# Kernel optimization log

Measured on AMD Instinct MI355X. Metric: run time of the kernel, lower is better.

## Reference

```python
import jax, jax.numpy as jnp
import numpy as np

D_MODEL = 1024
N_HEADS = 16  # long-term branch; short/medium use N_HEADS // 2


def _band_bias(seq_len, scale_factor):
    # Intended semantics of create_temporal_mask: position i may attend to
    # positions j >= i - scale_factor (recent past + all future); positions
    # further than scale_factor in the past are blocked.
    i = jnp.arange(seq_len)[:, None]
    j = jnp.arange(seq_len)[None, :]
    return jnp.where(j >= i - scale_factor, 0.0, -1e9).astype(jnp.float32)


def _mha(x, w_in, b_in, w_out, b_out, n_heads, bias):
    # Faithful nn.MultiheadAttention (batch_first, eval/no dropout).
    B, S, D = x.shape
    dk = D // n_heads
    qkv = x @ w_in.T + b_in                       # [B,S,3D]
    q, k, v = jnp.split(qkv, 3, axis=-1)
    def heads(t):
        return t.reshape(B, S, n_heads, dk).transpose(0, 2, 1, 3)  # [B,H,S,dk]
    q, k, v = heads(q), heads(k), heads(v)
    scores = jnp.einsum('bhid,bhjd->bhij', q, k) / np.sqrt(dk).astype(np.float32)
    if bias is not None:
        scores = scores + bias
    attn = jax.nn.softmax(scores, axis=-1)        # [B,H,S,S]
    out = jnp.einsum('bhij,bhjd->bhid', attn, v)  # [B,H,S,dk]
    out = out.transpose(0, 2, 1, 3).reshape(B, S, D)
    return out @ w_out.T + b_out, attn


def _layernorm(x, gamma, beta, eps=1e-5):
    mu = jnp.mean(x, axis=-1, keepdims=True)
    var = jnp.var(x, axis=-1, keepdims=True)
    return (x - mu) * jax.lax.rsqrt(var + eps) * gamma + beta


def setup_inputs() -> dict:
    key = jax.random.key(0)
    ks = jax.random.split(key, 12)
    D = D_MODEL
    s = 0.02
    inp = {
        'x': jax.random.normal(ks[0], (2, 2048, D), dtype=jnp.float32),
        'w_in_s': jax.random.normal(ks[1], (3 * D, D), dtype=jnp.float32) * s,
        'b_in_s': jnp.zeros((3 * D,), dtype=jnp.float32),
        'wo_s': jax.random.normal(ks[2], (D, D), dtype=jnp.float32) * s,
        'bo_s': jnp.zeros((D,), dtype=jnp.float32),
        'w_in_m': jax.random.normal(ks[3], (3 * D, D), dtype=jnp.float32) * s,
        'b_in_m': jnp.zeros((3 * D,), dtype=jnp.float32),
        'wo_m': jax.random.normal(ks[4], (D, D), dtype=jnp.float32) * s,
        'bo_m': jnp.zeros((D,), dtype=jnp.float32),
        'w_in_l': jax.random.normal(ks[5], (3 * D, D), dtype=jnp.float32) * s,
        'b_in_l': jnp.zeros((3 * D,), dtype=jnp.float32),
        'wo_l': jax.random.normal(ks[6], (D, D), dtype=jnp.float32) * s,
        'bo_l': jnp.zeros((D,), dtype=jnp.float32),
        'w_comb': jax.random.normal(ks[7], (D, 3 * D), dtype=jnp.float32) * s,
        'b_comb': jnp.zeros((D,), dtype=jnp.float32),
        'gamma': jnp.ones((D,), dtype=jnp.float32),
        'beta': jnp.zeros((D,), dtype=jnp.float32),
    }
    return inp


def reference(x, w_in_s, b_in_s, wo_s, bo_s,
              w_in_m, b_in_m, wo_m, bo_m,
              w_in_l, b_in_l, wo_l, bo_l,
              w_comb, b_comb, gamma, beta):
    B, S, D = x.shape
    short_bias = _band_bias(S, 10)
    medium_bias = _band_bias(S, 30)
    short_out, _ = _mha(x, w_in_s, b_in_s, wo_s, bo_s, N_HEADS // 2, short_bias)
    medium_out, _ = _mha(x, w_in_m, b_in_m, wo_m, bo_m, N_HEADS // 2, medium_bias)
    long_out, attn = _mha(x, w_in_l, b_in_l, wo_l, bo_l, N_HEADS, None)
    attn_weights = jnp.mean(attn, axis=1)  # torch default average_attn_weights=True -> [B,S,S]
    combined = jnp.concatenate([short_out, medium_out, long_out], axis=-1)
    output = combined @ w_comb.T + b_comb
    return _layernorm(output + x, gamma, beta), attn_weights
```

## Files before the change

kernel.cpp:

```cpp
#include <hip/hip_runtime.h>
#include <hip/hip_bf16.h>
#include <math.h>

#define B_ 2
#define S_ 2048
#define D_ 1024
#define M_ (B_*S_)
#define CTXLD 3072

typedef _Float16 half8_t __attribute__((ext_vector_type(8)));
typedef _Float16 half4_t __attribute__((ext_vector_type(4)));
typedef float    f32x4  __attribute__((ext_vector_type(4)));

#define GL2LDS(g, l) __builtin_amdgcn_global_load_lds( \
    (const __attribute__((address_space(1))) void*)(uintptr_t)(g), \
    (__attribute__((address_space(3))) void*)(l), 16, 0, 0)

#define QSC_L  0.18033688011112043f
#define QSC_SM 0.12751744653921766f

struct GemmBatch {
    const _Float16* A;
    const _Float16* W;
    const float*    bias;
    void*           C;
    void*           C2;
};

template<int MODE, int NB>
__global__ __launch_bounds__(256) void gemm_f16(
    GemmBatch b0, GemmBatch b1, GemmBatch b2, int lda, int ldw, int ldc, int K)
{
    constexpr int NT = NB / 32;
    __shared__ __align__(16) _Float16 As[2*128*32];
    __shared__ __align__(16) _Float16 Bs[2*NB*32];

    const GemmBatch G = (blockIdx.z == 0) ? b0 : ((blockIdx.z == 1) ? b1 : b2);

    const int t = threadIdx.x, lane = t & 63, w = t >> 6;
    const int bm = blockIdx.x * 128, bn = blockIdx.y * NB;
    const int wm = (w >> 1) * 64, wn = (w & 1) * (NB/2);
    const int fr = lane & 15, q8 = (lane >> 4) * 8;
    const int srow = lane >> 2, scol = (lane & 3) * 8;

    f32x4 acc[4][NT] = {};

    const _Float16* Ab = G.A + (size_t)(bm + w*32 + srow) * lda + scol;
    const _Float16* Wb = G.W + (size_t)(bn + w*(NB/4) + srow) * ldw + scol;

    for (int k0 = 0; k0 < K; k0 += 64) {
        __syncthreads();
        #pragma unroll
        for (int kc = 0; kc < 2; kc++) {
            #pragma unroll
            for (int ii = 0; ii < 2; ii++)
                GL2LDS(Ab + (size_t)(ii*16)*lda + k0 + kc*32,
                       As + kc*4096 + w*1024 + ii*512);
            #pragma unroll
            for (int ii = 0; ii < NB/64; ii++)
                GL2LDS(Wb + (size_t)(ii*16)*ldw + k0 + kc*32,
                       Bs + kc*NB*32 + w*(NB/4)*32 + ii*512);
        }
        __syncthreads();
        #pragma unroll
        for (int kc = 0; kc < 2; kc++) {
            half8_t af[4], bf[NT];
            #pragma unroll
            for (int mt = 0; mt < 4; mt++)
                af[mt] = *(const half8_t*)&As[kc*4096 + (wm + mt*16 + fr)*32 + q8];
            #pragma unroll
            for (int nt = 0; nt < NT; nt++)
                bf[nt] = *(const half8_t*)&Bs[kc*NB*32 + (wn + nt*16 + fr)*32 + q8];
            #pragma unroll
            for (int mt = 0; mt < 4; mt++)
                #pragma unroll
                for (int nt = 0; nt < NT; nt++)
                    acc[mt][nt] = __builtin_amdgcn_mfma_f32_16x16x32_f16(
                        af[mt], bf[nt], acc[mt][nt], 0, 0, 0);
        }
    }

    const int cl = lane & 15;
    const int rq = (lane >> 4) * 4;

    if (MODE == 2 && bn >= 2048) {
        #pragma unroll
        for (int mt = 0; mt < 4; mt++) {
            int row0 = bm + wm + mt*16 + rq;
            #pragma unroll
            for (int nt = 0; nt < NT; nt++) {
                int gcol = bn + wn + nt*16 + cl;
                float bv = G.bias[gcol];
                half4_t hv = {(_Float16)(acc[mt][nt][0] + bv),
                              (_Float16)(acc[mt][nt][1] + bv),
                              (_Float16)(acc[mt][nt][2] + bv),
                              (_Float16)(acc[mt][nt][3] + bv)};
                *(half4_t*)((_Float16*)G.C2 + (size_t)(gcol - 2048) * M_ + row0) = hv;
            }
        }
        return;
    }

    const float qsc = (MODE == 2 && bn < 1024)
                      ? ((blockIdx.z == 2) ? QSC_L : QSC_SM) : 1.0f;

    #pragma unroll
    for (int mt = 0; mt < 4; mt++) {
        #pragma unroll
        for (int r = 0; r < 4; r++) {
            size_t grow = (size_t)(bm + wm + mt*16 + rq + r);
            #pragma unroll
            for (int nt = 0; nt < NT; nt++) {
                int gcol = bn + wn + nt*16 + cl;
                float v = acc[mt][nt][r] + ((MODE == 3) ? 0.f : G.bias[gcol]);
                if (MODE == 2) v *= qsc;
                if (MODE == 0)
                    ((float*)G.C)[grow * ldc + gcol] = v;
                else
                    ((_Float16*)G.C)[grow * ldc + gcol] = (_Float16)v;
            }
        }
    }
}

struct CastArgs {
    const float* s[5];
    _Float16*    d[5];
    int          nb[5];
};

__global__ __launch_bounds__(256) void cast_all(CastArgs a)
{
    int off = blockIdx.x;
    int seg = 0;
    while (seg < 4 && off >= a.nb[seg]) { off -= a.nb[seg]; seg++; }
    int i = off * 256 + threadIdx.x;
    float4 v = ((const float4*)a.s[seg])[i];
    half4_t h = {(_Float16)v.x, (_Float16)v.y, (_Float16)v.z, (_Float16)v.w};
    ((half4_t*)a.d[seg])[i] = h;
}

__global__ __launch_bounds__(256) void transpose_cast_wo(
    const float* s0, const float* s1, const float* s2,
    _Float16* d0, _Float16* d1, _Float16* d2)
{
    __shared__ float T[64][68];
    const float* src = blockIdx.z == 0 ? s0 : (blockIdx.z == 1 ? s1 : s2);
    _Float16*    dst = blockIdx.z == 0 ? d0 : (blockIdx.z == 1 ? d1 : d2);
    const int db = blockIdx.x * 64;
    const int eb = blockIdx.y * 64;
    const int r = threadIdx.x >> 4;
    const int c = (threadIdx.x & 15) * 4;

    #pragma unroll
    for (int rr = 0; rr < 4; rr++) {
        float4 v = *(const float4*)&src[(size_t)(db + rr*16 + r)*1024 + eb + c];
        T[rr*16 + r][c+0] = v.x; T[rr*16 + r][c+1] = v.y;
        T[rr*16 + r][c+2] = v.z; T[rr*16 + r][c+3] = v.w;
    }
    __syncthreads();
    #pragma unroll
    for (int rr = 0; rr < 4; rr++) {
        int e = rr*16 + r;
        half4_t hv = {(_Float16)T[c+0][e], (_Float16)T[c+1][e],
                      (_Float16)T[c+2][e], (_Float16)T[c+3][e]};
        *(half4_t*)&dst[(size_t)(eb + e)*1024 + db + c] = hv;
    }
}

__global__ __launch_bounds__(256) void beff_kernel(
    const float* __restrict__ w_comb, const float* __restrict__ b_comb,
    const float* __restrict__ bo_s, const float* __restrict__ bo_m,
    const float* __restrict__ bo_l, float* __restrict__ beff)
{
    __shared__ float red[4];
    const int n = blockIdx.x, t = threadIdx.x;
    float s = 0.f;
    for (int d = t; d < 1024; d += 256)
        s += w_comb[(size_t)n*3072 + d]        * bo_s[d]
           + w_comb[(size_t)n*3072 + 1024 + d] * bo_m[d]
           + w_comb[(size_t)n*3072 + 2048 + d] * bo_l[d];
    #pragma unroll
    for (int m = 32; m >= 1; m >>= 1) s += __shfl_xor(s, m);
    if ((t & 63) == 0) red[t >> 6] = s;
    __syncthreads();
    if (t == 0) beff[n] = b_comb[n] + red[0] + red[1] + red[2] + red[3];
}

template<int DK, int BJ, bool LOUT>
__device__ __forceinline__ void flash_body(
    _Float16* lds, float* Lw,
    const _Float16* __restrict__ qk, const _Float16* __restrict__ vT,
    _Float16* __restrict__ ctx, float* __restrict__ lout,
    int window, int b, int h, int qblk, int H)
{
    constexpr int KS  = DK / 32;
    constexpr int DT  = DK / 16;
    constexpr int JT  = BJ / 16;
    constexpr int JC  = BJ / 32;
    constexpr int LDP = 40;

    _Float16* Ks = lds;
    _Float16* Vs = lds + DK*BJ;
    _Float16* Ps = lds + 2*DK*BJ;

    const int t = threadIdx.x, lane = t & 63, w = t >> 6;
    const int fr = lane & 15, g = lane >> 4, k8 = g * 8;
    const int k8s = (g ^ ((fr >> 1) & 3)) * 8;
    const int blkQ = qblk * 64;
    const int qlo  = blkQ + w * 16;

    _Float16* PsW = Ps + w * 16 * LDP;
    const int srow = lane >> 2;
    const int ssw  = ((lane & 3) ^ ((srow >> 1) & 3)) * 8;

    half8_t qf[KS];
    #pragma unroll
    for (int kk = 0; kk < KS; kk++)
        qf[kk] = *(const half8_t*)&qk[(size_t)(b*S_ + qlo + fr)*2048 + h*DK + kk*32 + k8];

    f32x4 O[DT] = {};
    float lsum = 0.f;

    for (int j0 = 0; j0 < S_; j0 += BJ) {
        if (window >= 0 && j0 + BJ - 1 < blkQ - window) continue;
        __syncthreads();

        #pragma unroll
        for (int kk = 0; kk < KS; kk++)
            #pragma unroll
            for (int ii = 0; ii < BJ/64; ii++)
                GL2LDS(&qk[(size_t)(b*S_ + j0 + w*(BJ/4) + ii*16 + srow)*2048
                           + 1024 + h*DK + kk*32 + ssw],
                       &Ks[kk*BJ*32 + w*(BJ/4)*32 + ii*512]);
        #pragma unroll
        for (int jc = 0; jc < JC; jc++)
            #pragma unroll
            for (int ii = 0; ii < DK/64; ii++)
                GL2LDS(&vT[(size_t)(h*DK + w*(DK/4) + ii*16 + srow)*M_
                           + b*S_ + j0 + jc*32 + ssw],
                       &Vs[jc*DK*32 + w*(DK/4)*32 + ii*512]);
        __syncthreads();

        f32x4 st[JT];
        #pragma unroll
        for (int jt = 0; jt < JT; jt++) {
            f32x4 s = {};
            #pragma unroll
            for (int kk = 0; kk < KS; kk++) {
                half8_t kf = *(const half8_t*)&Ks[kk*BJ*32 + (jt*16 + fr)*32 + k8s];
                s = __builtin_amdgcn_mfma_f32_16x16x32_f16(kf, qf[kk], s, 0, 0, 0);
            }
            st[jt] = s;
        }

        const bool full = (window < 0) || (j0 >= qlo + 15 - window);
        #pragma unroll
        for (int kc = 0; kc < JC; kc++) {
            #pragma unroll
            for (int jh = 0; jh < 2; jh++) {
                int jt = kc*2 + jh;
                float p[4];
                #pragma unroll
                for (int r = 0; r < 4; r++) {
                    float pv = exp2f(st[jt][r]);
                    if (!full) {
                        int jg = j0 + jt*16 + g*4 + r;
                        if (jg < (qlo + fr) - window) pv = 0.f;
                    }
                    p[r] = pv;
                    lsum += pv;
                }
                half4_t ph = {(_Float16)p[0], (_Float16)p[1],
                              (_Float16)p[2], (_Float16)p[3]};
                *(half4_t*)&PsW[fr*LDP + jh*16 + g*4] = ph;
            }
            half8_t pf = *(const half8_t*)&PsW[fr*LDP + k8];
            #pragma unroll
            for (int dt = 0; dt < DT; dt++) {
                half8_t vf = *(const half8_t*)&Vs[kc*DK*32 + (dt*16 + fr)*32 + k8s];
                O[dt] = __builtin_amdgcn_mfma_f32_16x16x32_f16(pf, vf, O[dt], 0, 0, 0);
            }
        }
    }

    lsum += __shfl_xor(lsum, 16);
    lsum += __shfl_xor(lsum, 32);
    if (g == 0) Lw[w*16 + fr] = lsum;
    float linv[4];
    #pragma unroll
    for (int r = 0; r < 4; r++)
        linv[r] = 1.f / Lw[w*16 + g*4 + r];

    if (LOUT && g == 0)
        lout[(size_t)(b*H + h)*S_ + qlo + fr] = lsum;

    #pragma unroll
    for (int r = 0; r < 4; r++) {
        _Float16* cp = ctx + (size_t)(b*S_ + qlo + g*4 + r)*CTXLD + h*DK;
        #pragma unroll
        for (int dt = 0; dt < DT; dt++)
            cp[dt*16 + fr] = (_Float16)(O[dt][r] * linv[r]);
    }
}

__global__ __launch_bounds__(256, 4) void flash_mega(
    const _Float16* __restrict__ qk_s, const _Float16* __restrict__ qk_m,
    const _Float16* __restrict__ qk_l,
    const _Float16* __restrict__ vT_s, const _Float16* __restrict__ vT_m,
    const _Float16* __restrict__ vT_l,
    _Float16* __restrict__ ctxall, float* __restrict__ lbuf)
{
    __shared__ __align__(16) _Float16 lds[18944];
    __shared__ float Lw[64];

    const int hwb = blockIdx.x;
    const int bid = (hwb & 7) * 256 + (hwb >> 3);
    if (bid < 1024) {
        int qblk = bid & 31, h = (bid >> 5) & 15, b = bid >> 9;
        flash_body<64, 128, true>(lds, Lw, qk_l, vT_l, ctxall + 2048, lbuf,
                                  -1, b, h, qblk, 16);
    } else {
        int r = bid - 1024;
        int qblk = r & 31;
        int h = (r >> 5) & 7;
        int z = r >> 8;
        int br = z >> 1, b = z & 1;
        flash_body<128, 64, false>(lds, Lw, br ? qk_m : qk_s, br ? vT_m : vT_s,
                                   ctxall + (br ? 1024 : 0), nullptr,
                                   br ? 30 : 10, b, h, qblk, 8);
    }
}

__global__ __launch_bounds__(256, 4) void attn_mean3(
    const _Float16* __restrict__ qk,
    const float* __restrict__ lbuf,
    float* __restrict__ attn)
{
    __shared__ __align__(16) _Float16 Ks[2 * 2 * 128 * 32];

    const int t = threadIdx.x, lane = t & 63, w = t >> 6;
    const int fr = lane & 15, g = lane >> 4, k8 = g * 8;
    const int k8s = (g ^ ((fr >> 1) & 3)) * 8;
    const int j0 = blockIdx.x * 128;
    const int irow = blockIdx.y * 64 + w * 16;
    const int b = blockIdx.z;
    const int srow = lane >> 2;
    const int ssw  = ((lane & 3) ^ ((srow >> 1) & 3)) * 8;

    f32x4 acc[8] = {};

    for (int hp = 0; hp < 16; hp += 2) {
        __syncthreads();
        #pragma unroll
        for (int hh = 0; hh < 2; hh++)
            #pragma unroll
            for (int kk = 0; kk < 2; kk++)
                #pragma unroll
                for (int ii = 0; ii < 2; ii++)
                    GL2LDS(&qk[(size_t)(b*S_ + j0 + w*32 + ii*16 + srow)*2048
                               + 1024 + (hp+hh)*64 + kk*32 + ssw],
                           &Ks[hh*8192 + kk*4096 + w*1024 + ii*512]);
        __syncthreads();

        #pragma unroll
        for (int hh = 0; hh < 2; hh++) {
            const int h = hp + hh;
            half8_t af[2];
            #pragma unroll
            for (int kk = 0; kk < 2; kk++)
                af[kk] = *(const half8_t*)
                    &qk[(size_t)(b*S_ + irow + fr)*2048 + h*64 + kk*32 + k8];

            float lg[4];
            #pragma unroll
            for (int r = 0; r < 4; r++)
                lg[r] = __log2f(lbuf[(size_t)(b*16 + h)*S_ + irow + g*4 + r]) + 4.0f;

            #pragma unroll
            for (int nt = 0; nt < 8; nt++) {
                f32x4 s = {};
                #pragma unroll
                for (int kk = 0; kk < 2; kk++) {
                    half8_t bf = *(const half8_t*)
                        &Ks[hh*8192 + kk*4096 + (nt*16 + fr)*32 + k8s];
                    s = __builtin_amdgcn_mfma_f32_16x16x32_f16(af[kk], bf, s, 0, 0, 0);
                }
                #pragma unroll
                for (int r = 0; r < 4; r++)
                    acc[nt][r] += exp2f(s[r] - lg[r]);
            }
        }
    }

    #pragma unroll
    for (int r = 0; r < 4; r++) {
        float* p = attn + (size_t)(b*S_ + irow + g*4 + r)*S_ + j0;
        #pragma unroll
        for (int nt = 0; nt < 8; nt++)
            p[nt*16 + fr] = acc[nt][r];
    }
}

__global__ __launch_bounds__(256) void ln_residual(
    const float* __restrict__ pre, const float* __restrict__ x,
    const float* __restrict__ gamma, const float* __restrict__ beta,
    float* __restrict__ out)
{
    __shared__ float redS[4], redQ[4];
    const int row = blockIdx.x;
    const int t = threadIdx.x;
    size_t base = (size_t)row * D_ + t * 4;

    float4 v  = *(const float4*)(pre + base);
    float4 xv = *(const float4*)(x + base);
    v.x += xv.x; v.y += xv.y; v.z += xv.z; v.w += xv.w;

    float s = v.x + v.y + v.z + v.w;
    float q = v.x*v.x + v.y*v.y + v.z*v.z + v.w*v.w;
    #pragma unroll
    for (int m = 32; m >= 1; m >>= 1) {
        s += __shfl_xor(s, m);
        q += __shfl_xor(q, m);
    }
    int wave = t >> 6;
    if ((t & 63) == 0) { redS[wave] = s; redQ[wave] = q; }
    __syncthreads();
    s = redS[0] + redS[1] + redS[2] + redS[3];
    q = redQ[0] + redQ[1] + redQ[2] + redQ[3];

    float mean = s * (1.f / D_);
    float var  = q * (1.f / D_) - mean * mean;
    float rstd = rsqrtf(var + 1e-5f);

    float4 g  = *(const float4*)(gamma + t * 4);
    float4 be = *(const float4*)(beta + t * 4);
    float4 o;
    o.x = (v.x - mean) * rstd * g.x + be.x;
    o.y = (v.y - mean) * rstd * g.y + be.y;
    o.z = (v.z - mean) * rstd * g.z + be.z;
    o.w = (v.w - mean) * rstd * g.w + be.w;
    *(float4*)(out + base) = o;
}

extern "C" void kernel_launch(void* const* d_in, const int* in_sizes, int n_in,
                              void* d_out, int out_size, void* d_ws, size_t ws_size,
                              hipStream_t stream)
{
    (void)in_sizes; (void)n_in; (void)out_size; (void)ws_size;
    const float* x      = (const float*)d_in[0];
    const float* w_in_s = (const float*)d_in[1];
    const float* b_in_s = (const float*)d_in[2];
    const float* wo_s   = (const float*)d_in[3];
    const float* bo_s   = (const float*)d_in[4];
    const float* w_in_m = (const float*)d_in[5];
    const float* b_in_m = (const float*)d_in[6];
    const float* wo_m   = (const float*)d_in[7];
    const float* bo_m   = (const float*)d_in[8];
    const float* w_in_l = (const float*)d_in[9];
    const float* b_in_l = (const float*)d_in[10];
    const float* wo_l   = (const float*)d_in[11];
    const float* bo_l   = (const float*)d_in[12];
    const float* w_comb = (const float*)d_in[13];
    const float* b_comb = (const float*)d_in[14];
    const float* gamma  = (const float*)d_in[15];
    const float* beta   = (const float*)d_in[16];

    float* out    = (float*)d_out;
    float* attn_o = out + (size_t)M_ * D_;

    char* W = (char*)d_ws;
    _Float16* w_in_s_h = (_Float16*)(W);
    _Float16* w_in_m_h = (_Float16*)(W + 6291456);
    _Float16* w_in_l_h = (_Float16*)(W + 12582912);
    _Float16* w_comb_h = (_Float16*)(W + 18874368);
    _Float16* woT_s    = (_Float16*)(W + 25165824);
    _Float16* woT_m    = (_Float16*)(W + 27262976);
    _Float16* woT_l    = (_Float16*)(W + 29360128);
    _Float16* weff     = (_Float16*)(W + 31457280);
    _Float16* qk_s     = (_Float16*)(W + 37748736);
    _Float16* qk_m     = (_Float16*)(W + 54525952);
    _Float16* qk_l     = (_Float16*)(W + 71303168);
    _Float16* vT_s     = (_Float16*)(W + 88080384);
    _Float16* vT_m     = (_Float16*)(W + 96468992);
    _Float16* ctxall   = (_Float16*)(W + 104857600);
    _Float16* x_h      = (_Float16*)(W + 130023424);
    float*    lbuf     = (float*)   (W + 138412032);
    float*    beff     = (float*)   (W + 138674432);
    _Float16* vT_l     = w_comb_h;
    float*    pre      = (float*)qk_m;

    dim3 blk(256);
    GemmBatch nil = { nullptr, nullptr, nullptr, nullptr, nullptr };

    CastArgs ca;
    ca.s[0]=x;      ca.d[0]=x_h;      ca.nb[0]=4096;
    ca.s[1]=w_in_s; ca.d[1]=w_in_s_h; ca.nb[1]=3072;
    ca.s[2]=w_in_m; ca.d[2]=w_in_m_h; ca.nb[2]=3072;
    ca.s[3]=w_in_l; ca.d[3]=w_in_l_h; ca.nb[3]=3072;
    ca.s[4]=w_comb; ca.d[4]=w_comb_h; ca.nb[4]=3072;
    cast_all<<<dim3(16384), blk, 0, stream>>>(ca);

    transpose_cast_wo<<<dim3(16, 16, 3), blk, 0, stream>>>(
        wo_s, wo_m, wo_l, woT_s, woT_m, woT_l);

    GemmBatch we0 = { w_comb_h + 0,    woT_s, nullptr, weff + 0,    nullptr };
    GemmBatch we1 = { w_comb_h + 1024, woT_m, nullptr, weff + 1024, nullptr };
    GemmBatch we2 = { w_comb_h + 2048, woT_l, nullptr, weff + 2048, nullptr };
    gemm_f16<3, 64><<<dim3(8, 16, 3), blk, 0, stream>>>(we0, we1, we2, 3072, 1024, 3072, 1024);

    beff_kernel<<<dim3(1024), blk, 0, stream>>>(w_comb, b_comb, bo_s, bo_m, bo_l, beff);

    GemmBatch qs = { x_h, w_in_s_h, b_in_s, qk_s, vT_s };
    GemmBatch qm = { x_h, w_in_m_h, b_in_m, qk_m, vT_m };
    GemmBatch ql = { x_h, w_in_l_h, b_in_l, qk_l, vT_l };
    gemm_f16<2, 128><<<dim3(M_/128, 3072/128, 3), blk, 0, stream>>>(qs, qm, ql, D_, D_, 2048, D_);

    flash_mega<<<dim3(2048), blk, 0, stream>>>(
        qk_s, qk_m, qk_l, vT_s, vT_m, vT_l, ctxall, lbuf);

    attn_mean3<<<dim3(S_/128, S_/64, B_), blk, 0, stream>>>(qk_l, lbuf, attn_o);

    GemmBatch fb = { ctxall, weff, beff, pre, nullptr };
    gemm_f16<0, 64><<<dim3(M_/128, 1024/64, 1), blk, 0, stream>>>(fb, nil, nil, 3072, 3072, D_, 3072);

    ln_residual<<<dim3(M_), blk, 0, stream>>>(pre, x, gamma, beta, out);
}
```

Before: 527.5 us.

## Merge prep kernels and co-schedule final GEMM with attention-mean kernel

Folds the cast, transpose-cast and effective-bias kernels into one prep launch dispatched by block index. It also runs the final combine GEMM and the attention-weight mean computation in a single tail launch that shares one LDS buffer. The aim is to cut launch overhead and let two independent workloads fill the GPU together instead of running back to back. The cost is that the tail kernel's LDS footprint and launch bounds now cover both bodies, which may change occupancy for the GEMM part.

```diff
diff --git a/kernel.cpp b/kernel.cpp
--- a/kernel.cpp
+++ b/kernel.cpp
@@ -28,17 +28,14 @@
 };
 
 template<int MODE, int NB>
-__global__ __launch_bounds__(256) void gemm_f16(
-    GemmBatch b0, GemmBatch b1, GemmBatch b2, int lda, int ldw, int ldc, int K)
+__device__ __forceinline__ void gemm_body(
+    _Float16* As, _Float16* Bs, const GemmBatch& G,
+    int lda, int ldw, int ldc, int K, int bx, int by, int bz)
 {
     constexpr int NT = NB / 32;
-    __shared__ __align__(16) _Float16 As[2*128*32];
-    __shared__ __align__(16) _Float16 Bs[2*NB*32];
-
-    const GemmBatch G = (blockIdx.z == 0) ? b0 : ((blockIdx.z == 1) ? b1 : b2);
 
     const int t = threadIdx.x, lane = t & 63, w = t >> 6;
-    const int bm = blockIdx.x * 128, bn = blockIdx.y * NB;
+    const int bm = bx * 128, bn = by * NB;
     const int wm = (w >> 1) * 64, wn = (w & 1) * (NB/2);
     const int fr = lane & 15, q8 = (lane >> 4) * 8;
     const int srow = lane >> 2, scol = (lane & 3) * 8;
@@ -102,7 +99,7 @@
     }
 
     const float qsc = (MODE == 2 && bn < 1024)
-                      ? ((blockIdx.z == 2) ? QSC_L : QSC_SM) : 1.0f;
+                      ? ((bz == 2) ? QSC_L : QSC_SM) : 1.0f;
 
     #pragma unroll
     for (int mt = 0; mt < 4; mt++) {
@@ -123,68 +120,85 @@
     }
 }
 
+template<int MODE, int NB>
+__global__ __launch_bounds__(256) void gemm_f16(
+    GemmBatch b0, GemmBatch b1, GemmBatch b2, int lda, int ldw, int ldc, int K)
+{
+    __shared__ __align__(16) _Float16 As[2*128*32];
+    __shared__ __align__(16) _Float16 Bs[2*NB*32];
+    const GemmBatch G = (blockIdx.z == 0) ? b0 : ((blockIdx.z == 1) ? b1 : b2);
+    gemm_body<MODE, NB>(As, Bs, G, lda, ldw, ldc, K,
+                        blockIdx.x, blockIdx.y, blockIdx.z);
+}
+
 struct CastArgs {
     const float* s[5];
     _Float16*    d[5];
     int          nb[5];
 };
 
-__global__ __launch_bounds__(256) void cast_all(CastArgs a)
-{
-    int off = blockIdx.x;
-    int seg = 0;
-    while (seg < 4 && off >= a.nb[seg]) { off -= a.nb[seg]; seg++; }
-    int i = off * 256 + threadIdx.x;
-    float4 v = ((const float4*)a.s[seg])[i];
-    half4_t h = {(_Float16)v.x, (_Float16)v.y, (_Float16)v.z, (_Float16)v.w};
-    ((half4_t*)a.d[seg])[i] = h;
-}
-
-__global__ __launch_bounds__(256) void transpose_cast_wo(
-    const float* s0, const float* s1, const float* s2,
-    _Float16* d0, _Float16* d1, _Float16* d2)
-{
-    __shared__ float T[64][68];
-    const float* src = blockIdx.z == 0 ? s0 : (blockIdx.z == 1 ? s1 : s2);
-    _Float16*    dst = blockIdx.z == 0 ? d0 : (blockIdx.z == 1 ? d1 : d2);
-    const int db = blockIdx.x * 64;
-    const int eb = blockIdx.y * 64;
-    const int r = threadIdx.x >> 4;
-    const int c = (threadIdx.x & 15) * 4;
-
-    #pragma unroll
-    for (int rr = 0; rr < 4; rr++) {
-        float4 v = *(const float4*)&src[(size_t)(db + rr*16 + r)*1024 + eb + c];
-        T[rr*16 + r][c+0] = v.x; T[rr*16 + r][c+1] = v.y;
-        T[rr*16 + r][c+2] = v.z; T[rr*16 + r][c+3] = v.w;
-    }
-    __syncthreads();
-    #pragma unroll
-    for (int rr = 0; rr < 4; rr++) {
-        int e = rr*16 + r;
-        half4_t hv = {(_Float16)T[c+0][e], (_Float16)T[c+1][e],
-                      (_Float16)T[c+2][e], (_Float16)T[c+3][e]};
-        *(half4_t*)&dst[(size_t)(eb + e)*1024 + db + c] = hv;
-    }
-}
-
-__global__ __launch_bounds__(256) void beff_kernel(
+__global__ __launch_bounds__(256) void prep_mega(
+    CastArgs a,
+    const float* wo_s, const float* wo_m, const float* wo_l,
+    _Float16* woT_s, _Float16* woT_m, _Float16* woT_l,
     const float* __restrict__ w_comb, const float* __restrict__ b_comb,
     const float* __restrict__ bo_s, const float* __restrict__ bo_m,
     const float* __restrict__ bo_l, float* __restrict__ beff)
 {
+    __shared__ float T[64][68];
     __shared__ float red[4];
-    const int n = blockIdx.x, t = threadIdx.x;
-    float s = 0.f;
-    for (int d = t; d < 1024; d += 256)
-        s += w_comb[(size_t)n*3072 + d]        * bo_s[d]
-           + w_comb[(size_t)n*3072 + 1024 + d] * bo_m[d]
-           + w_comb[(size_t)n*3072 + 2048 + d] * bo_l[d];
-    #pragma unroll
-    for (int m = 32; m >= 1; m >>= 1) s += __shfl_xor(s, m);
-    if ((t & 63) == 0) red[t >> 6] = s;
-    __syncthreads();
-    if (t == 0) beff[n] = b_comb[n] + red[0] + red[1] + red[2] + red[3];
+    const int bid = blockIdx.x;
+
+    if (bid < 16384) {
+        int off = bid;
+        int seg = 0;
+        while (seg < 4 && off >= a.nb[seg]) { off -= a.nb[seg]; seg++; }
+        int i = off * 256 + threadIdx.x;
+        float4 v = ((const float4*)a.s[seg])[i];
+        half4_t h = {(_Float16)v.x, (_Float16)v.y, (_Float16)v.z, (_Float16)v.w};
+        ((half4_t*)a.d[seg])[i] = h;
+        return;
+    }
+    if (bid < 16384 + 768) {
+        int rr0 = bid - 16384;
+        int bz = rr0 >> 8, rem = rr0 & 255;
+        int bx = rem & 15, by = rem >> 4;
+        const float* src = bz == 0 ? wo_s : (bz == 1 ? wo_m : wo_l);
+        _Float16*    dst = bz == 0 ? woT_s : (bz == 1 ? woT_m : woT_l);
+        const int db = bx * 64;
+        const int eb = by * 64;
+        const int r = threadIdx.x >> 4;
+        const int c = (threadIdx.x & 15) * 4;
+
+        #pragma unroll
+        for (int rr = 0; rr < 4; rr++) {
+            float4 v = *(const float4*)&src[(size_t)(db + rr*16 + r)*1024 + eb + c];
+            T[rr*16 + r][c+0] = v.x; T[rr*16 + r][c+1] = v.y;
+            T[rr*16 + r][c+2] = v.z; T[rr*16 + r][c+3] = v.w;
+        }
+        __syncthreads();
+        #pragma unroll
+        for (int rr = 0; rr < 4; rr++) {
+            int e = rr*16 + r;
+            half4_t hv = {(_Float16)T[c+0][e], (_Float16)T[c+1][e],
+                          (_Float16)T[c+2][e], (_Float16)T[c+3][e]};
+            *(half4_t*)&dst[(size_t)(eb + e)*1024 + db + c] = hv;
+        }
+        return;
+    }
+    {
+        const int n = bid - (16384 + 768), t = threadIdx.x;
+        float s = 0.f;
+        for (int d = t; d < 1024; d += 256)
+            s += w_comb[(size_t)n*3072 + d]        * bo_s[d]
+               + w_comb[(size_t)n*3072 + 1024 + d] * bo_m[d]
+               + w_comb[(size_t)n*3072 + 2048 + d] * bo_l[d];
+        #pragma unroll
+        for (int m = 32; m >= 1; m >>= 1) s += __shfl_xor(s, m);
+        if ((t & 63) == 0) red[t >> 6] = s;
+        __syncthreads();
+        if (t == 0) beff[n] = b_comb[n] + red[0] + red[1] + red[2] + red[3];
+    }
 }
 
 template<int DK, int BJ, bool LOUT>
@@ -332,19 +346,17 @@
     }
 }
 
-__global__ __launch_bounds__(256, 4) void attn_mean3(
+__device__ __forceinline__ void attn_mean_body(
+    _Float16* Ks,
     const _Float16* __restrict__ qk,
     const float* __restrict__ lbuf,
-    float* __restrict__ attn)
-{
-    __shared__ __align__(16) _Float16 Ks[2 * 2 * 128 * 32];
-
+    float* __restrict__ attn, int bx, int by, int b)
+{
     const int t = threadIdx.x, lane = t & 63, w = t >> 6;
     const int fr = lane & 15, g = lane >> 4, k8 = g * 8;
     const int k8s = (g ^ ((fr >> 1) & 3)) * 8;
-    const int j0 = blockIdx.x * 128;
-    const int irow = blockIdx.y * 64 + w * 16;
-    const int b = blockIdx.z;
+    const int j0 = bx * 128;
+    const int irow = by * 64 + w * 16;
     const int srow = lane >> 2;
     const int ssw  = ((lane & 3) ^ ((srow >> 1) & 3)) * 8;
 
@@ -399,6 +411,23 @@
         #pragma unroll
         for (int nt = 0; nt < 8; nt++)
             p[nt*16 + fr] = acc[nt][r];
+    }
+}
+
+__global__ __launch_bounds__(256, 4) void tail_mega(
+    GemmBatch fb, const _Float16* __restrict__ qk_l,
+    const float* __restrict__ lbuf, float* __restrict__ attn_o)
+{
+    __shared__ __align__(16) _Float16 lds[16384];
+
+    const int bid = blockIdx.x;
+    if (bid < 512) {
+        gemm_body<0, 64>(lds, lds + 8192, fb,
+                         3072, 3072, D_, 3072, bid & 31, bid >> 5, 0);
+    } else {
+        int r = bid - 512;
+        attn_mean_body(lds, qk_l, lbuf, attn_o,
+                       r & 15, (r >> 4) & 31, r >> 9);
     }
 }
 
@@ -499,18 +528,15 @@
     ca.s[2]=w_in_m; ca.d[2]=w_in_m_h; ca.nb[2]=3072;
     ca.s[3]=w_in_l; ca.d[3]=w_in_l_h; ca.nb[3]=3072;
     ca.s[4]=w_comb; ca.d[4]=w_comb_h; ca.nb[4]=3072;
-    cast_all<<<dim3(16384), blk, 0, stream>>>(ca);
-
-    transpose_cast_wo<<<dim3(16, 16, 3), blk, 0, stream>>>(
-        wo_s, wo_m, wo_l, woT_s, woT_m, woT_l);
+    prep_mega<<<dim3(16384 + 768 + 1024), blk, 0, stream>>>(
+        ca, wo_s, wo_m, wo_l, woT_s, woT_m, woT_l,
+        w_comb, b_comb, bo_s, bo_m, bo_l, beff);
 
     GemmBatch we0 = { w_comb_h + 0,    woT_s, nullptr, weff + 0,    nullptr };
     GemmBatch we1 = { w_comb_h + 1024, woT_m, nullptr, weff + 1024, nullptr };
     GemmBatch we2 = { w_comb_h + 2048, woT_l, nullptr, weff + 2048, nullptr };
     gemm_f16<3, 64><<<dim3(8, 16, 3), blk, 0, stream>>>(we0, we1, we2, 3072, 1024, 3072, 1024);
 
-    beff_kernel<<<dim3(1024), blk, 0, stream>>>(w_comb, b_comb, bo_s, bo_m, bo_l, beff);
-
     GemmBatch qs = { x_h, w_in_s_h, b_in_s, qk_s, vT_s };
     GemmBatch qm = { x_h, w_in_m_h, b_in_m, qk_m, vT_m };
     GemmBatch ql = { x_h, w_in_l_h, b_in_l, qk_l, vT_l };
@@ -519,10 +545,8 @@
     flash_mega<<<dim3(2048), blk, 0, stream>>>(
         qk_s, qk_m, qk_l, vT_s, vT_m, vT_l, ctxall, lbuf);
 
-    attn_mean3<<<dim3(S_/128, S_/64, B_), blk, 0, stream>>>(qk_l, lbuf, attn_o);
-
     GemmBatch fb = { ctxall, weff, beff, pre, nullptr };
-    gemm_f16<0, 64><<<dim3(M_/128, 1024/64, 1), blk, 0, stream>>>(fb, nil, nil, 3072, 3072, D_, 3072);
+    tail_mega<<<dim3(512 + 1024), blk, 0, stream>>>(fb, qk_l, lbuf, attn_o);
 
     ln_residual<<<dim3(M_), blk, 0, stream>>>(pre, x, gamma, beta, out);
 }
```

Result: no change. 517.7 us (-1.8%).
